# Kernel tuning notes

Measured on AMD Instinct MI355X. Metric: run time of the kernel, lower is better.

Reference implementation:

```python
import jax, jax.numpy as jnp
import numpy as np

MAXK = 5

def _l2norm(x, axis):
    return x / jnp.maximum(jnp.linalg.norm(x, axis=axis, keepdims=True), 1e-12)

def _conv3x3(x, w, b):
    y = jax.lax.conv_general_dilated(x, w, (1, 1), [(1, 1), (1, 1)],
                                     dimension_numbers=('NCHW', 'OIHW', 'NCHW'))
    return y + b[None, :, None, None]

def _bilinear_resize(img, oh, ow):
    # img: [C, ih, iw]; torch F.interpolate(mode='bilinear', align_corners=False)
    ih, iw = img.shape[-2], img.shape[-1]
    def co(o, i):
        src = jnp.clip((jnp.arange(o, dtype=jnp.float32) + 0.5) * (i / o) - 0.5, 0.0, i - 1.0)
        i0 = jnp.floor(src).astype(jnp.int32)
        i1 = jnp.minimum(i0 + 1, i - 1)
        return i0, i1, src - i0
    y0, y1, wy = co(oh, ih)
    x0, x1, wx = co(ow, iw)
    a = img[:, y0][:, :, x0]; b = img[:, y0][:, :, x1]
    c = img[:, y1][:, :, x0]; d = img[:, y1][:, :, x1]
    top = a * (1 - wx) + b * wx
    bot = c * (1 - wx) + d * wx
    return top * (1 - wy[:, None]) + bot * wy[:, None]

def _pos_encode(x, ms, w, b):
    n, _, h, wd = x.shape
    lin = jnp.linspace(-1.0, 1.0, ms)
    gx, gy = jnp.meshgrid(lin, lin, indexing='ij')
    pg = _bilinear_resize(jnp.stack([gx, gy], 0), h, wd)  # [2, h, wd]
    return x + _conv3x3(jnp.broadcast_to(pg[None], (n, 2, h, wd)), w, b)

def _unfold(x, k, s, p):
    # torch F.unfold ordering: channel index = c*k*k + i*k + j
    n, c, h, w = x.shape
    xp = jnp.pad(x, ((0, 0), (0, 0), (p, p), (p, p)))
    oh = (h + 2 * p - k) // s + 1
    ow = (w + 2 * p - k) // s + 1
    cols = [xp[:, :, i:i + oh * s:s, j:j + ow * s:s] for i in range(k) for j in range(k)]
    return jnp.stack(cols, 2).reshape(n, c * k * k, oh * ow)

def _fold(t, c, k, s, p, out_h, out_w):
    n = t.shape[0]
    oh = (out_h + 2 * p - k) // s + 1
    ow = (out_w + 2 * p - k) // s + 1
    pt = t.reshape(n, c, k, k, oh, ow)
    out = jnp.zeros((n, c, out_h + 2 * p, out_w + 2 * p), t.dtype)
    for i in range(k):
        for j in range(k):
            out = out.at[:, :, i:i + oh * s:s, j:j + ow * s:s].add(pt[:, :, i, j])
    return out[:, :, p:p + out_h, p:p + out_w]

def _se(x, w1, b1, w2, b2):
    y = x.mean((2, 3))
    y = jax.nn.sigmoid(jax.nn.relu(y @ w1.T + b1) @ w2.T + b2)
    return x * y[:, :, None, None]

def reference(lrsr_lv3, refsr_lv3, ref_lv1, ref_lv2, ref_lv3,
              k_logits, temperature, global_weight,
              pos_w1, pos_b1, pos_w2, pos_b2, pos_w3, pos_b3,
              se1_w1, se1_b1, se1_w2, se1_b2,
              se2_w1, se2_b1, se2_w2, se2_b2,
              se3_w1, se3_b1, se3_w2, se3_b2):
    N, C, H, W = lrsr_lv3.shape
    HW = H * W
    refsr_enc = _pos_encode(refsr_lv3, 64, pos_w3, pos_b3)
    refsr_n = _l2norm(_unfold(refsr_enc, 3, 1, 1).transpose(0, 2, 1), 2)  # [N, HW, C*9]
    lrsr_n = _l2norm(_unfold(lrsr_lv3, 3, 1, 1), 1)                        # [N, C*9, HW]
    R_local = refsr_n @ lrsr_n                                             # [N, HW, HW]
    ref_g = _l2norm(refsr_enc.mean((2, 3)), 1)
    lr_g = _l2norm(lrsr_lv3.mean((2, 3)), 1)
    R_glob = jnp.sum(ref_g * lr_g, 1)[:, None, None]
    R_comb = (1.0 - global_weight) * R_local + global_weight * R_glob
    # DynamicKSelector: gumbel-softmax with fixed noise key for determinism
    u = jax.random.uniform(jax.random.key(42), k_logits.shape, jnp.float32, 1e-6, 1.0)
    g = -jnp.log(-jnp.log(u))
    k_probs = jax.nn.softmax((k_logits + g) / temperature, -1)
    k_hard = jnp.argmax(k_probs, -1) + 1  # [num_levels]
    # topk(max_k) once; per-level mask with -inf values / 0 indices == original pad
    vals, idx = jax.lax.top_k(R_comb.transpose(0, 2, 1), MAXK)  # [N, HW, K]
    R_star_full = vals.transpose(0, 2, 1)  # [N, K, HW]
    R_idx_full = idx.transpose(0, 2, 1)

    def transfer(ref_feat, lvl, ms, pw, pb, kern, s, p):
        rf = _pos_encode(ref_feat, ms, pw, pb)
        ru = _unfold(rf, kern, s, p)  # [N, C*kern^2, HW]
        mask = (jnp.arange(MAXK) < k_hard[lvl])[None, :, None]
        Rs = jnp.where(mask, R_star_full, -jnp.inf)  # sigmoid(-inf)=0 -> padded rows vanish
        Ri = jnp.where(mask, R_idx_full, 0)
        T_all = jnp.zeros((N, ru.shape[1], HW), ru.dtype)
        for i in range(MAXK):  # small fixed loop over k candidates
            sel = jnp.take_along_axis(ru, Ri[:, i][:, None, :], axis=2)
            T_all = T_all + sel * jax.nn.sigmoid(Rs[:, i])[:, None, :]
        return _fold(T_all, ref_feat.shape[1], kern, s, p, H * s, W * s) / float(kern * kern)

    T3 = transfer(ref_lv3, 0, 64, pos_w3, pos_b3, 3, 1, 1)
    T2 = transfer(ref_lv2, 1, 128, pos_w2, pos_b2, 6, 2, 2)
    T1 = transfer(ref_lv1, 2, 256, pos_w1, pos_b1, 12, 4, 4)
    T3 = _se(T3, se3_w1, se3_b1, se3_w2, se3_b2)
    T2 = _se(T2, se2_w1, se2_b1, se2_w2, se2_b2)
    T1 = _se(T1, se1_w1, se1_b1, se1_w2, se1_b2)
    return (T3, T2, T1)

def setup_inputs():
    key = jax.random.key(0)
    ks = jax.random.split(key, 16)
    N, H, W = 2, 48, 48
    f = jnp.float32
    d = {}
    d['lrsr_lv3'] = jax.random.normal(ks[0], (N, 256, H, W), f)
    d['refsr_lv3'] = jax.random.normal(ks[1], (N, 256, H, W), f)
    d['ref_lv1'] = jax.random.normal(ks[2], (N, 64, 4 * H, 4 * W), f)
    d['ref_lv2'] = jax.random.normal(ks[3], (N, 128, 2 * H, 2 * W), f)
    d['ref_lv3'] = jax.random.normal(ks[4], (N, 256, H, W), f)
    d['k_logits'] = jax.random.normal(ks[5], (3, 5), f)
    d['temperature'] = jnp.array(1.0, f)
    d['global_weight'] = jnp.array(0.1, f)
    for nm, c, i in [('1', 64, 6), ('2', 128, 7), ('3', 256, 8)]:
        d['pos_w' + nm] = jax.random.normal(ks[i], (c, 2, 3, 3), f) * 0.01
        d['pos_b' + nm] = jnp.zeros((c,), f)
    for nm, c, i in [('1', 64, 9), ('2', 128, 10), ('3', 256, 11)]:
        r = c // 16
        k1, k2 = jax.random.split(ks[i])
        d['se' + nm + '_w1'] = jax.random.normal(k1, (r, c), f) / np.sqrt(c).astype(np.float32)
        d['se' + nm + '_b1'] = jnp.zeros((r,), f)
        d['se' + nm + '_w2'] = jax.random.normal(k2, (c, r), f) / np.sqrt(r).astype(np.float32)
        d['se' + nm + '_b2'] = jnp.zeros((c,), f)
    return d
```

## Files before the change

kernel.cpp:

```cpp
#include <hip/hip_runtime.h>
#include <cstdint>
#include <cmath>

#define HW48 2304
#define F9   2304

typedef _Float16 half8_t __attribute__((ext_vector_type(8)));
typedef float floatx4 __attribute__((ext_vector_type(4)));

__global__ void enc_kernel(const float* __restrict__ src, const float* __restrict__ w,
                           const float* __restrict__ b, float* __restrict__ dst,
                           int C, int H, int ms, int total) {
  int idx = blockIdx.x * blockDim.x + threadIdx.x;
  if (idx >= total) return;
  int x = idx % H;
  int y = (idx / H) % H;
  int c = (idx / (H * H)) % C;
  float scale = (float)((double)ms / (double)H);
  float msm1 = (float)(ms - 1);
  float conv = b[c];
#pragma unroll
  for (int dy = 0; dy < 3; ++dy) {
    int yy = y + dy - 1;
    if (yy < 0 || yy >= H) continue;
    float sy = fminf(fmaxf((yy + 0.5f) * scale - 0.5f, 0.0f), msm1);
    float g0 = -1.0f + 2.0f * sy / msm1;
#pragma unroll
    for (int dx = 0; dx < 3; ++dx) {
      int xx = x + dx - 1;
      if (xx < 0 || xx >= H) continue;
      float sx = fminf(fmaxf((xx + 0.5f) * scale - 0.5f, 0.0f), msm1);
      float g1 = -1.0f + 2.0f * sx / msm1;
      conv += w[((c * 2 + 0) * 3 + dy) * 3 + dx] * g0
            + w[((c * 2 + 1) * 3 + dy) * 3 + dx] * g1;
    }
  }
  dst[idx] = src[idx] + conv;
}

__global__ void unfold_norm_kernel(const float* __restrict__ src,
                                   _Float16* __restrict__ dhi,
                                   _Float16* __restrict__ dlo) {
  int pos = blockIdx.x;
  int n = blockIdx.y;
  int y = pos / 48, x = pos - (pos / 48) * 48;
  int tid = threadIdx.x;
  const float* s = src + (size_t)n * 256 * HW48;
  float v[9];
  float ss = 0.0f;
#pragma unroll
  for (int it = 0; it < 9; ++it) {
    int f = tid + it * 256;
    int c = f / 9, r = f - c * 9;
    int dy = r / 3, dx = r - dy * 3;
    int yy = y + dy - 1, xx = x + dx - 1;
    float val = 0.0f;
    if (yy >= 0 && yy < 48 && xx >= 0 && xx < 48)
      val = s[(c * 48 + yy) * 48 + xx];
    v[it] = val;
    ss += val * val;
  }
  __shared__ float red[256];
  red[tid] = ss;
  __syncthreads();
  for (int ofs = 128; ofs > 0; ofs >>= 1) {
    if (tid < ofs) red[tid] += red[tid + ofs];
    __syncthreads();
  }
  float norm = fmaxf(sqrtf(red[0]), 1e-12f);
  _Float16* dh = dhi + ((size_t)n * HW48 + pos) * (size_t)F9;
  _Float16* dl = dlo + ((size_t)n * HW48 + pos) * (size_t)F9;
#pragma unroll
  for (int it = 0; it < 9; ++it) {
    int f = tid + it * 256;
    float xv = v[it] / norm;
    _Float16 h = (_Float16)xv;
    dh[f] = h;
    dl[f] = (_Float16)(xv - (float)h);
  }
}

__global__ void chmean_kernel(const float* __restrict__ src, float* __restrict__ out, int C, int HW) {
  int c = blockIdx.x, n = blockIdx.y;
  const float* s = src + ((size_t)n * C + c) * HW;
  float sum = 0.0f;
  for (int i = threadIdx.x; i < HW; i += blockDim.x) sum += s[i];
  __shared__ float red[256];
  red[threadIdx.x] = sum;
  __syncthreads();
  for (int ofs = 128; ofs > 0; ofs >>= 1) {
    if (threadIdx.x < ofs) red[threadIdx.x] += red[threadIdx.x + ofs];
    __syncthreads();
  }
  if (threadIdx.x == 0) out[n * C + c] = red[0] / (float)HW;
}

__global__ void rglob_kernel(const float* __restrict__ mref, const float* __restrict__ mlr,
                             float* __restrict__ rg) {
  int n = blockIdx.x;
  int tid = threadIdx.x;
  float a = mref[n * 256 + tid];
  float b = mlr[n * 256 + tid];
  __shared__ float raa[256], rbb[256], rab[256];
  raa[tid] = a * a; rbb[tid] = b * b; rab[tid] = a * b;
  __syncthreads();
  for (int ofs = 128; ofs > 0; ofs >>= 1) {
    if (tid < ofs) { raa[tid] += raa[tid + ofs]; rbb[tid] += rbb[tid + ofs]; rab[tid] += rab[tid + ofs]; }
    __syncthreads();
  }
  if (tid == 0) {
    float na = fmaxf(sqrtf(raa[0]), 1e-12f);
    float nb = fmaxf(sqrtf(rbb[0]), 1e-12f);
    rg[n] = rab[0] / (na * nb);
  }
}

__device__ inline unsigned rotl32(unsigned v, int r) { return (v << r) | (v >> (32 - r)); }

__global__ void khard_kernel(const float* __restrict__ k_logits, const float* __restrict__ temp,
                             int* __restrict__ kh) {
  if (threadIdx.x != 0 || blockIdx.x != 0) return;
  const unsigned ksa[3] = {0u, 42u, 0u ^ 42u ^ 0x1BD11BDAu};
  const int R0[4] = {13, 15, 26, 6};
  const int R1[4] = {17, 29, 16, 24};
  float T = temp[0];
  for (int lvl = 0; lvl < 3; ++lvl) {
    int best = 0;
    float bv = -1e30f;
    for (int j = 0; j < 5; ++j) {
      int idx = lvl * 5 + j;
      unsigned x0 = 0u + ksa[0];
      unsigned x1 = (unsigned)idx + ksa[1];
      for (int grp = 0; grp < 5; ++grp) {
        const int* rr = (grp & 1) ? R1 : R0;
        for (int q = 0; q < 4; ++q) { x0 += x1; x1 = rotl32(x1, rr[q]); x1 ^= x0; }
        x0 += ksa[(grp + 1) % 3];
        x1 += ksa[(grp + 2) % 3] + (unsigned)(grp + 1);
      }
      unsigned bb = x0 ^ x1;
      float f = __uint_as_float((bb >> 9) | 0x3f800000u) - 1.0f;
      float u = __fadd_rn(__fmul_rn(f, 1.0f - 1e-6f), 1e-6f);
      u = fmaxf(u, 1e-6f);
      float g = -logf(-logf(u));
      float v = (k_logits[idx] + g) / T;
      if (v > bv) { bv = v; best = j; }
    }
    kh[lvl] = best + 1;
  }
}

#define LDH 40
__global__ __launch_bounds__(256) void gemm_mfma_kernel(
    const _Float16* __restrict__ Ah, const _Float16* __restrict__ Al,
    const _Float16* __restrict__ Bh, const _Float16* __restrict__ Bl,
    float* __restrict__ C, const float* __restrict__ rg, const float* __restrict__ gwp) {
  __shared__ __align__(16) _Float16 As_h[128 * LDH];
  __shared__ __align__(16) _Float16 As_l[128 * LDH];
  __shared__ __align__(16) _Float16 Bs_h[128 * LDH];
  __shared__ __align__(16) _Float16 Bs_l[128 * LDH];
  const int n = blockIdx.z;
  const size_t nb = (size_t)n * HW48 * F9;
  const _Float16* Ahp = Ah + nb + (size_t)(blockIdx.y * 128) * F9;
  const _Float16* Alp = Al + nb + (size_t)(blockIdx.y * 128) * F9;
  const _Float16* Bhp = Bh + nb + (size_t)(blockIdx.x * 128) * F9;
  const _Float16* Blp = Bl + nb + (size_t)(blockIdx.x * 128) * F9;
  const int tid = threadIdx.x;
  const int lane = tid & 63, wid = tid >> 6;
  const int wm = (wid >> 1) * 64, wn = (wid & 1) * 64;
  const int r16 = lane & 15, quad = lane >> 4;

  floatx4 acc[4][4];
#pragma unroll
  for (int i = 0; i < 4; ++i)
#pragma unroll
    for (int j = 0; j < 4; ++j) acc[i][j] = (floatx4){0.f, 0.f, 0.f, 0.f};

  for (int k0 = 0; k0 < F9; k0 += 32) {
#pragma unroll
    for (int u = 0; u < 2; ++u) {
      int slot = tid + 256 * u;
      int row = slot >> 2, ch = slot & 3;
      size_t goff = (size_t)row * F9 + k0 + ch * 8;
      int loff = row * LDH + ch * 8;
      *(float4*)&As_h[loff] = *(const float4*)&Ahp[goff];
      *(float4*)&As_l[loff] = *(const float4*)&Alp[goff];
      *(float4*)&Bs_h[loff] = *(const float4*)&Bhp[goff];
      *(float4*)&Bs_l[loff] = *(const float4*)&Blp[goff];
    }
    __syncthreads();
    half8_t ah[4], al[4], bh[4], bl[4];
#pragma unroll
    for (int i = 0; i < 4; ++i) {
      int ra = (wm + i * 16 + r16) * LDH + quad * 8;
      ah[i] = *(const half8_t*)&As_h[ra];
      al[i] = *(const half8_t*)&As_l[ra];
      int rb = (wn + i * 16 + r16) * LDH + quad * 8;
      bh[i] = *(const half8_t*)&Bs_h[rb];
      bl[i] = *(const half8_t*)&Bs_l[rb];
    }
#pragma unroll
    for (int i = 0; i < 4; ++i)
#pragma unroll
      for (int j = 0; j < 4; ++j) {
        acc[i][j] = __builtin_amdgcn_mfma_f32_16x16x32_f16(ah[i], bh[j], acc[i][j], 0, 0, 0);
        acc[i][j] = __builtin_amdgcn_mfma_f32_16x16x32_f16(ah[i], bl[j], acc[i][j], 0, 0, 0);
        acc[i][j] = __builtin_amdgcn_mfma_f32_16x16x32_f16(al[i], bh[j], acc[i][j], 0, 0, 0);
      }
    __syncthreads();
  }
  float gw = gwp[0];
  float base = gw * rg[n];
  float w1 = 1.0f - gw;
  float* Cp = C + (size_t)n * HW48 * HW48;
#pragma unroll
  for (int i = 0; i < 4; ++i) {
#pragma unroll
    for (int j = 0; j < 4; ++j) {
#pragma unroll
      for (int r = 0; r < 4; ++r) {
        int row = blockIdx.y * 128 + wm + i * 16 + quad * 4 + r;
        int col = blockIdx.x * 128 + wn + j * 16 + r16;
        Cp[(size_t)row * HW48 + col] = w1 * acc[i][j][r] + base;
      }
    }
  }
}

__global__ __launch_bounds__(256) void topk_kernel(const float* __restrict__ R,
                                                   float* __restrict__ Wsig,
                                                   int* __restrict__ Pidx) {
  const int n = blockIdx.y;
  const int tq = threadIdx.x & 15;
  const int tp = threadIdx.x >> 4;
  const int q = blockIdx.x * 16 + tq;
  const float* Rp = R + (size_t)n * HW48 * HW48 + q;
  float v0 = -3.0e38f, v1 = v0, v2 = v0, v3 = v0, v4 = v0;
  int i0 = 0, i1 = 0, i2 = 0, i3 = 0, i4 = 0;
  const int pbeg = tp * 144, pend = pbeg + 144;
  for (int p = pbeg; p < pend; ++p) {
    float val = Rp[(size_t)p * HW48];
    if (val > v4) {
      if (val > v0)      { v4=v3;i4=i3; v3=v2;i3=i2; v2=v1;i2=i1; v1=v0;i1=i0; v0=val;i0=p; }
      else if (val > v1) { v4=v3;i4=i3; v3=v2;i3=i2; v2=v1;i2=i1; v1=val;i1=p; }
      else if (val > v2) { v4=v3;i4=i3; v3=v2;i3=i2; v2=val;i2=p; }
      else if (val > v3) { v4=v3;i4=i3; v3=val;i3=p; }
      else               { v4=val;i4=p; }
    }
  }
  __shared__ float cv[16][16][5];
  __shared__ int   ci[16][16][5];
  cv[tq][tp][0] = v0; ci[tq][tp][0] = i0;
  cv[tq][tp][1] = v1; ci[tq][tp][1] = i1;
  cv[tq][tp][2] = v2; ci[tq][tp][2] = i2;
  cv[tq][tp][3] = v3; ci[tq][tp][3] = i3;
  cv[tq][tp][4] = v4; ci[tq][tp][4] = i4;
  __syncthreads();
  if (tp == 0) {
    float w0 = -3.0e38f, w1 = w0, w2 = w0, w3 = w0, w4 = w0;
    int j0 = 0, j1 = 0, j2 = 0, j3 = 0, j4 = 0;
    for (int s = 0; s < 16; ++s) {
#pragma unroll
      for (int j = 0; j < 5; ++j) {
        float val = cv[tq][s][j];
        int   pi  = ci[tq][s][j];
        if (val > w4) {
          if (val > w0)      { w4=w3;j4=j3; w3=w2;j3=j2; w2=w1;j2=j1; w1=w0;j1=j0; w0=val;j0=pi; }
          else if (val > w1) { w4=w3;j4=j3; w3=w2;j3=j2; w2=w1;j2=j1; w1=val;j1=pi; }
          else if (val > w2) { w4=w3;j4=j3; w3=w2;j3=j2; w2=val;j2=pi; }
          else if (val > w3) { w4=w3;j4=j3; w3=val;j3=pi; }
          else               { w4=val;j4=pi; }
        }
      }
    }
    size_t o = ((size_t)n * HW48 + q) * 5;
    Wsig[o + 0] = 1.0f / (1.0f + expf(-w0)); Pidx[o + 0] = j0;
    Wsig[o + 1] = 1.0f / (1.0f + expf(-w1)); Pidx[o + 1] = j1;
    Wsig[o + 2] = 1.0f / (1.0f + expf(-w2)); Pidx[o + 2] = j2;
    Wsig[o + 3] = 1.0f / (1.0f + expf(-w3)); Pidx[o + 3] = j3;
    Wsig[o + 4] = 1.0f / (1.0f + expf(-w4)); Pidx[o + 4] = j4;
  }
}

__global__ void transfer_kernel(const float* __restrict__ refenc, const float* __restrict__ Wsig,
                                const int* __restrict__ Pidx, const int* __restrict__ khp,
                                float* __restrict__ out, int C, int s, int pad, int lvl,
                                float kk, int total) {
  int idx = blockIdx.x * blockDim.x + threadIdx.x;
  if (idx >= total) return;
  int Hout = 48 * s;
  int X = idx % Hout;
  int Y = (idx / Hout) % Hout;
  int c = (idx / (Hout * Hout)) % C;
  int n = idx / (C * Hout * Hout);
  int kh = khp[lvl];
  int Yp = Y + pad, Xp = X + pad;
  int Qy = Yp / s, Qx = Xp / s;
  const float* rf = refenc + ((size_t)n * C + c) * (size_t)(Hout * Hout);
  const float* Wq = Wsig + (size_t)n * HW48 * 5;
  const int* Pq = Pidx + (size_t)n * HW48 * 5;
  float acc = 0.0f;
  for (int t = 0; t < 3; ++t) {
    int qh = Qy - t;
    if (qh < 0 || qh >= 48) continue;
    int i = Yp - s * qh;
    for (int u = 0; u < 3; ++u) {
      int qw = Qx - u;
      if (qw < 0 || qw >= 48) continue;
      int j = Xp - s * qw;
      int q = qh * 48 + qw;
      for (int m = 0; m < kh; ++m) {
        float wgt = Wq[q * 5 + m];
        int p = Pq[q * 5 + m];
        int ph = p / 48, pw = p - (p / 48) * 48;
        int yy = ph * s + i - pad;
        int xx = pw * s + j - pad;
        if (yy >= 0 && yy < Hout && xx >= 0 && xx < Hout)
          acc += wgt * rf[yy * Hout + xx];
      }
    }
  }
  out[idx] = acc / kk;
}

__global__ void se_mlp_kernel(const float* __restrict__ means, const float* __restrict__ w1,
                              const float* __restrict__ b1, const float* __restrict__ w2,
                              const float* __restrict__ b2, float* __restrict__ scale,
                              int C, int R) {
  int n = blockIdx.x;
  int tid = threadIdx.x;
  __shared__ float ym[256];
  __shared__ float h1[16];
  if (tid < C) ym[tid] = means[n * C + tid];
  __syncthreads();
  if (tid < R) {
    float s = b1[tid];
    for (int c = 0; c < C; ++c) s += ym[c] * w1[tid * C + c];
    h1[tid] = fmaxf(s, 0.0f);
  }
  __syncthreads();
  if (tid < C) {
    float s = b2[tid];
    for (int r = 0; r < R; ++r) s += h1[r] * w2[tid * R + r];
    scale[n * C + tid] = 1.0f / (1.0f + expf(-s));
  }
}

__global__ void se_scale_kernel(float* __restrict__ T, const float* __restrict__ scale,
                                int C, int HW, int total) {
  int idx = blockIdx.x * blockDim.x + threadIdx.x;
  if (idx >= total) return;
  int c = (idx / HW) % C;
  int n = idx / (C * HW);
  T[idx] *= scale[n * C + c];
}

extern "C" void kernel_launch(void* const* d_in, const int* in_sizes, int n_in,
                              void* d_out, int out_size, void* d_ws, size_t ws_size,
                              hipStream_t stream) {
  const float* lrsr   = (const float*)d_in[0];
  const float* refsr  = (const float*)d_in[1];
  const float* ref1   = (const float*)d_in[2];
  const float* ref2   = (const float*)d_in[3];
  const float* ref3   = (const float*)d_in[4];
  const float* klog   = (const float*)d_in[5];
  const float* temp   = (const float*)d_in[6];
  const float* gwp    = (const float*)d_in[7];
  const float* pos_w1 = (const float*)d_in[8];
  const float* pos_b1 = (const float*)d_in[9];
  const float* pos_w2 = (const float*)d_in[10];
  const float* pos_b2 = (const float*)d_in[11];
  const float* pos_w3 = (const float*)d_in[12];
  const float* pos_b3 = (const float*)d_in[13];
  const float* se1_w1 = (const float*)d_in[14];
  const float* se1_b1 = (const float*)d_in[15];
  const float* se1_w2 = (const float*)d_in[16];
  const float* se1_b2 = (const float*)d_in[17];
  const float* se2_w1 = (const float*)d_in[18];
  const float* se2_b1 = (const float*)d_in[19];
  const float* se2_w2 = (const float*)d_in[20];
  const float* se2_b2 = (const float*)d_in[21];
  const float* se3_w1 = (const float*)d_in[22];
  const float* se3_b1 = (const float*)d_in[23];
  const float* se3_w2 = (const float*)d_in[24];
  const float* se3_b2 = (const float*)d_in[25];
  float* out = (float*)d_out;
  float* ws = (float*)d_ws;

  float* refsr_enc = ws + 0;
  float* ref3_enc  = ws + 1179648;
  float* ref2_enc  = ws + 2359296;
  float* ref1_enc  = ws + 4718592;
  _Float16* Ah_hi  = (_Float16*)(ws + 9437184);
  _Float16* Ah_lo  = (_Float16*)(ws + 14745600);
  _Float16* Bh_hi  = (_Float16*)(ws + 20054016);
  _Float16* Bh_lo  = (_Float16*)(ws + 25362432);
  float* Rm        = ws + 30670848;
  float* Wsig      = ws + 41287680;
  int*   Pidx      = (int*)(ws + 41310720);
  float* mref      = ws + 41333760;
  float* mlr       = ws + 41334272;
  float* rg        = ws + 41334784;
  int*   kh        = (int*)(ws + 41334788);
  float* semean    = ws + 41334792;
  float* sescale   = ws + 41335304;

  float* T3 = out;
  float* T2 = out + 1179648;
  float* T1 = out + 3538944;

  enc_kernel<<<4608, 256, 0, stream>>>(refsr, pos_w3, pos_b3, refsr_enc, 256, 48, 64, 1179648);
  enc_kernel<<<4608, 256, 0, stream>>>(ref3, pos_w3, pos_b3, ref3_enc, 256, 48, 64, 1179648);
  enc_kernel<<<9216, 256, 0, stream>>>(ref2, pos_w2, pos_b2, ref2_enc, 128, 96, 128, 2359296);
  enc_kernel<<<18432, 256, 0, stream>>>(ref1, pos_w1, pos_b1, ref1_enc, 64, 192, 256, 4718592);

  unfold_norm_kernel<<<dim3(2304, 2), 256, 0, stream>>>(refsr_enc, Ah_hi, Ah_lo);
  unfold_norm_kernel<<<dim3(2304, 2), 256, 0, stream>>>(lrsr, Bh_hi, Bh_lo);

  chmean_kernel<<<dim3(256, 2), 256, 0, stream>>>(refsr_enc, mref, 256, 2304);
  chmean_kernel<<<dim3(256, 2), 256, 0, stream>>>(lrsr, mlr, 256, 2304);
  rglob_kernel<<<2, 256, 0, stream>>>(mref, mlr, rg);
  khard_kernel<<<1, 64, 0, stream>>>(klog, temp, kh);

  gemm_mfma_kernel<<<dim3(18, 18, 2), 256, 0, stream>>>(Ah_hi, Ah_lo, Bh_hi, Bh_lo, Rm, rg, gwp);

  topk_kernel<<<dim3(144, 2), 256, 0, stream>>>(Rm, Wsig, Pidx);

  transfer_kernel<<<4608, 256, 0, stream>>>(ref3_enc, Wsig, Pidx, kh, T3, 256, 1, 1, 0, 9.0f, 1179648);
  transfer_kernel<<<9216, 256, 0, stream>>>(ref2_enc, Wsig, Pidx, kh, T2, 128, 2, 2, 1, 36.0f, 2359296);
  transfer_kernel<<<18432, 256, 0, stream>>>(ref1_enc, Wsig, Pidx, kh, T1, 64, 4, 4, 2, 144.0f, 4718592);

  chmean_kernel<<<dim3(256, 2), 256, 0, stream>>>(T3, semean, 256, 2304);
  se_mlp_kernel<<<2, 256, 0, stream>>>(semean, se3_w1, se3_b1, se3_w2, se3_b2, sescale, 256, 16);
  se_scale_kernel<<<4608, 256, 0, stream>>>(T3, sescale, 256, 2304, 1179648);

  chmean_kernel<<<dim3(128, 2), 256, 0, stream>>>(T2, semean, 128, 9216);
  se_mlp_kernel<<<2, 256, 0, stream>>>(semean, se2_w1, se2_b1, se2_w2, se2_b2, sescale, 128, 8);
  se_scale_kernel<<<9216, 256, 0, stream>>>(T2, sescale, 128, 9216, 2359296);

  chmean_kernel<<<dim3(64, 2), 256, 0, stream>>>(T1, semean, 64, 36864);
  se_mlp_kernel<<<2, 256, 0, stream>>>(semean, se1_w1, se1_b1, se1_w2, se1_b2, sescale, 64, 4);
  se_scale_kernel<<<18432, 256, 0, stream>>>(T1, sescale, 64, 36864, 4718592);
}
```

Before: 1.156 ms.

## Amortize top-k index decoding across multiple channels per thread in transfer kernel

The transfer kernel now has each thread handle CV channels (4 or 8) for one spatial position, using a 3D grid over spatial, channel group and batch. The top-k weight and index loads and the patch coordinate arithmetic are therefore shared across channels instead of being repeated for each one. The top-k kernel also stores indices pre-split into packed (column, row) fields, so the per-use divide by 48 is no longer needed. The cost is more registers for the accumulator array, fewer threads launched, and strided loads across channel planes.

```diff
diff --git a/kernel.cpp b/kernel.cpp
--- a/kernel.cpp
+++ b/kernel.cpp
@@ -273,32 +273,37 @@
       }
     }
     size_t o = ((size_t)n * HW48 + q) * 5;
-    Wsig[o + 0] = 1.0f / (1.0f + expf(-w0)); Pidx[o + 0] = j0;
-    Wsig[o + 1] = 1.0f / (1.0f + expf(-w1)); Pidx[o + 1] = j1;
-    Wsig[o + 2] = 1.0f / (1.0f + expf(-w2)); Pidx[o + 2] = j2;
-    Wsig[o + 3] = 1.0f / (1.0f + expf(-w3)); Pidx[o + 3] = j3;
-    Wsig[o + 4] = 1.0f / (1.0f + expf(-w4)); Pidx[o + 4] = j4;
-  }
-}
-
-__global__ void transfer_kernel(const float* __restrict__ refenc, const float* __restrict__ Wsig,
-                                const int* __restrict__ Pidx, const int* __restrict__ khp,
-                                float* __restrict__ out, int C, int s, int pad, int lvl,
-                                float kk, int total) {
-  int idx = blockIdx.x * blockDim.x + threadIdx.x;
-  if (idx >= total) return;
-  int Hout = 48 * s;
-  int X = idx % Hout;
-  int Y = (idx / Hout) % Hout;
-  int c = (idx / (Hout * Hout)) % C;
-  int n = idx / (C * Hout * Hout);
+    Wsig[o + 0] = 1.0f / (1.0f + expf(-w0)); Pidx[o + 0] = ((j0 % 48) << 16) | (j0 / 48);
+    Wsig[o + 1] = 1.0f / (1.0f + expf(-w1)); Pidx[o + 1] = ((j1 % 48) << 16) | (j1 / 48);
+    Wsig[o + 2] = 1.0f / (1.0f + expf(-w2)); Pidx[o + 2] = ((j2 % 48) << 16) | (j2 / 48);
+    Wsig[o + 3] = 1.0f / (1.0f + expf(-w3)); Pidx[o + 3] = ((j3 % 48) << 16) | (j3 / 48);
+    Wsig[o + 4] = 1.0f / (1.0f + expf(-w4)); Pidx[o + 4] = ((j4 % 48) << 16) | (j4 / 48);
+  }
+}
+
+template<int CV>
+__global__ __launch_bounds__(256) void transfer_kernel(const float* __restrict__ refenc,
+                                                       const float* __restrict__ Wsig,
+                                                       const int* __restrict__ Pidx,
+                                                       const int* __restrict__ khp,
+                                                       float* __restrict__ out, int C, int s,
+                                                       int pad, int lvl, float kk) {
+  const int Hout = 48 * s;
+  const int HH = Hout * Hout;
+  int sp = blockIdx.x * 256 + threadIdx.x;
+  if (sp >= HH) return;
+  int X = sp % Hout, Y = sp / Hout;
+  int c0 = blockIdx.y * CV;
+  int n = blockIdx.z;
   int kh = khp[lvl];
   int Yp = Y + pad, Xp = X + pad;
   int Qy = Yp / s, Qx = Xp / s;
-  const float* rf = refenc + ((size_t)n * C + c) * (size_t)(Hout * Hout);
+  const float* rf = refenc + ((size_t)n * C + c0) * (size_t)HH;
   const float* Wq = Wsig + (size_t)n * HW48 * 5;
   const int* Pq = Pidx + (size_t)n * HW48 * 5;
-  float acc = 0.0f;
+  float acc[CV];
+#pragma unroll
+  for (int cv = 0; cv < CV; ++cv) acc[cv] = 0.0f;
   for (int t = 0; t < 3; ++t) {
     int qh = Qy - t;
     if (qh < 0 || qh >= 48) continue;
@@ -310,16 +315,23 @@
       int q = qh * 48 + qw;
       for (int m = 0; m < kh; ++m) {
         float wgt = Wq[q * 5 + m];
-        int p = Pq[q * 5 + m];
-        int ph = p / 48, pw = p - (p / 48) * 48;
+        int pxy = Pq[q * 5 + m];
+        int ph = pxy & 0xffff, pw = pxy >> 16;
         int yy = ph * s + i - pad;
         int xx = pw * s + j - pad;
-        if (yy >= 0 && yy < Hout && xx >= 0 && xx < Hout)
-          acc += wgt * rf[yy * Hout + xx];
+        if (yy >= 0 && yy < Hout && xx >= 0 && xx < Hout) {
+          const float* rp = rf + yy * Hout + xx;
+#pragma unroll
+          for (int cv = 0; cv < CV; ++cv)
+            acc[cv] = fmaf(wgt, rp[(size_t)cv * HH], acc[cv]);
+        }
       }
     }
   }
-  out[idx] = acc / kk;
+  float* op = out + ((size_t)n * C + c0) * (size_t)HH + sp;
+#pragma unroll
+  for (int cv = 0; cv < CV; ++cv)
+    op[(size_t)cv * HH] = acc[cv] / kk;
 }
 
 __global__ void se_mlp_kernel(const float* __restrict__ means, const float* __restrict__ w1,
@@ -425,9 +437,9 @@
 
   topk_kernel<<<dim3(144, 2), 256, 0, stream>>>(Rm, Wsig, Pidx);
 
-  transfer_kernel<<<4608, 256, 0, stream>>>(ref3_enc, Wsig, Pidx, kh, T3, 256, 1, 1, 0, 9.0f, 1179648);
-  transfer_kernel<<<9216, 256, 0, stream>>>(ref2_enc, Wsig, Pidx, kh, T2, 128, 2, 2, 1, 36.0f, 2359296);
-  transfer_kernel<<<18432, 256, 0, stream>>>(ref1_enc, Wsig, Pidx, kh, T1, 64, 4, 4, 2, 144.0f, 4718592);
+  transfer_kernel<4><<<dim3(9, 64, 2), 256, 0, stream>>>(ref3_enc, Wsig, Pidx, kh, T3, 256, 1, 1, 0, 9.0f);
+  transfer_kernel<8><<<dim3(36, 16, 2), 256, 0, stream>>>(ref2_enc, Wsig, Pidx, kh, T2, 128, 2, 2, 1, 36.0f);
+  transfer_kernel<8><<<dim3(144, 8, 2), 256, 0, stream>>>(ref1_enc, Wsig, Pidx, kh, T1, 64, 4, 4, 2, 144.0f);
 
   chmean_kernel<<<dim3(256, 2), 256, 0, stream>>>(T3, semean, 256, 2304);
   se_mlp_kernel<<<2, 256, 0, stream>>>(semean, se3_w1, se3_b1, se3_w2, se3_b2, sescale, 256, 16);
```

After: 1.268 ms. 1.1x slower.
